# Performance work log

Hardware: AMD Instinct MI355X
Metric: run time of the kernel (lower is better)

## Reference

```python
import jax, jax.numpy as jnp
import numpy as np

N = 100000   # num nodes / num_embs
D = 64       # dim
E = 1200000  # num edges (before self-loops)
L = 2        # num_layers
H = 1        # heads
EPS = 1e-5
NEG_SLOPE = 0.2


def setup_inputs() -> dict:
    key = jax.random.key(0)
    ks = jax.random.split(key, 12)
    return {
        "x": jax.random.normal(ks[0], (N, D), jnp.float32),  # unused by forward (matches torch)
        "edge_index": jax.random.randint(ks[1], (2, E), 0, N, dtype=jnp.int64),
        "emb_weight": jax.random.normal(ks[2], (N, D), jnp.float32) * 0.1,
        "ln_gamma": jnp.ones((L, D), jnp.float32),
        "ln_beta": jnp.zeros((L, D), jnp.float32),
        "Wl": jax.random.normal(ks[3], (L, D, H * D), jnp.float32) * 0.05,
        "Wr": jax.random.normal(ks[4], (L, D, H * D), jnp.float32) * 0.05,
        "att": jax.random.normal(ks[5], (L, H, D), jnp.float32) * 0.05,
        "conv_bias": jnp.zeros((L, D), jnp.float32),
        "post_w": jax.random.normal(ks[6], (D, D), jnp.float32) * 0.05,
        "post_b": jnp.zeros((D,), jnp.float32),
    }


def _layernorm(x, g, b):
    # pyg LayerNorm(mode='node'): per-node normalization over features
    mu = jnp.mean(x, axis=-1, keepdims=True)
    var = jnp.var(x, axis=-1, keepdims=True)
    return (x - mu) * jax.lax.rsqrt(var + EPS) * g + b


def _gatv2(x, src, tgt, Wl, Wr, a, bias):
    # x: [N, D]; Wl/Wr: [D, H*D]; a: [H, D]
    xl = (x @ Wl).reshape(N, H, D)  # source transform
    xr = (x @ Wr).reshape(N, H, D)  # target transform
    m = jax.nn.leaky_relu(xl[src] + xr[tgt], NEG_SLOPE)      # [Et, H, D]
    e = jnp.einsum('ehd,hd->eh', m, a)                       # [Et, H]
    # segment softmax over edges grouped by target node
    emax = jax.ops.segment_max(e, tgt, num_segments=N)       # [N, H]
    ex = jnp.exp(e - emax[tgt])
    denom = jax.ops.segment_sum(ex, tgt, num_segments=N)
    alpha = ex / (denom[tgt] + 1e-16)                        # [Et, H]
    out = jax.ops.segment_sum(xl[src] * alpha[..., None], tgt, num_segments=N)  # [N, H, D]
    return out.mean(axis=1) + bias                           # concat=False -> mean over heads


def reference(x, edge_index, emb_weight, ln_gamma, ln_beta, Wl, Wr, att, conv_bias, post_w, post_b):
    # GATv2Conv default add_self_loops=True
    loops = jnp.arange(N, dtype=edge_index.dtype)
    src = jnp.concatenate([edge_index[0], loops])
    tgt = jnp.concatenate([edge_index[1], loops])
    h = emb_weight  # forward replaces input x with embedding table
    for i in range(L):
        y = _layernorm(h, ln_gamma[i], ln_beta[i])
        y = _gatv2(y, src, tgt, Wl[i], Wr[i], att[i], conv_bias[i])
        y = jax.nn.gelu(y, approximate=False)
        h = y + h  # residual
    return h @ post_w + post_b
```

## Files before the change

### kernel.cpp

```cpp
#include <hip/hip_runtime.h>
#include <math.h>

#define NN 100000
#define DD 64
#define NE 1200000
#define NB 391
#define SCH 2048
#define GB ((NN + 63) / 64)
#define HS 88

typedef __attribute__((ext_vector_type(8))) short bf16x8;
typedef __attribute__((ext_vector_type(4))) float f32x4;

__device__ __forceinline__ unsigned short f2bf(float x) {
    unsigned u = __float_as_uint(x);
    return (unsigned short)((u + 0x7FFFu + ((u >> 16) & 1u)) >> 16);
}
__device__ __forceinline__ float bf2f(unsigned short b) {
    return __uint_as_float(((unsigned)b) << 16);
}

__device__ __forceinline__ float gelu_exact(float x) {
    return 0.5f * x * (1.0f + erff(x * 0.70710678118654752f));
}

__device__ __forceinline__ float leaky(float x) {
    return fmaxf(x, 0.f) + 0.2f * fminf(x, 0.f);
}


__global__ __launch_bounds__(256) void k_bcount(const int* __restrict__ tgt, int* __restrict__ bcnt) {
    __shared__ int h[NB];
    for (int i = threadIdx.x; i < NB; i += 256) h[i] = 0;
    __syncthreads();
    const int stride = gridDim.x * 256;
    for (int i = blockIdx.x * 256 + threadIdx.x; i < NE; i += stride)
        atomicAdd(&h[tgt[i] >> 8], 1);
    __syncthreads();
    for (int i = threadIdx.x; i < NB; i += 256)
        if (h[i]) atomicAdd(&bcnt[i], h[i]);
}

__global__ __launch_bounds__(512) void k_bscan(const int* __restrict__ bcnt,
                                               int* __restrict__ bbase, int* __restrict__ wbase) {
    __shared__ int s[512];
    const int tid = threadIdx.x;
    const int v = (tid < NB) ? bcnt[tid] : 0;
    s[tid] = v;
    __syncthreads();
    for (int o = 1; o < 512; o <<= 1) {
        int t = (tid >= o) ? s[tid - o] : 0;
        __syncthreads();
        s[tid] += t;
        __syncthreads();
    }
    if (tid < NB) {
        int ex = s[tid] - v;
        bbase[tid] = ex;
        wbase[tid] = ex;
    }
    if (tid == NB - 1) bbase[NB] = s[tid];
}

__global__ __launch_bounds__(256) void k_bscatter(const int* __restrict__ src, const int* __restrict__ tgt,
                                                  int* __restrict__ wbase, unsigned int* __restrict__ ebuf) {
    __shared__ int stgt[SCH];
    __shared__ unsigned short srk[SCH];
    __shared__ int hist[NB];
    __shared__ int hbase[NB];
    const int base = blockIdx.x * SCH;
    const int cnt = min(SCH, NE - base);
    const int tid = threadIdx.x;
    for (int i = tid; i < NB; i += 256) hist[i] = 0;
    for (int i = tid; i < cnt; i += 256) stgt[i] = tgt[base + i];
    __syncthreads();
    for (int i = tid; i < cnt; i += 256)
        srk[i] = (unsigned short)atomicAdd(&hist[stgt[i] >> 8], 1);
    __syncthreads();
    for (int b = tid; b < NB; b += 256) {
        int c = hist[b];
        hbase[b] = c ? atomicAdd(&wbase[b], c) : 0;
    }
    __syncthreads();
    for (int i = tid; i < cnt; i += 256) {
        int t = stgt[i];
        unsigned int e = ((unsigned int)src[base + i] << 8) | (unsigned int)(t & 255);
        ebuf[hbase[t >> 8] + (int)srk[i]] = e;
    }
}

__global__ __launch_bounds__(256) void k_bfinal(const int* __restrict__ bbase,
                                                const unsigned int* __restrict__ ebuf,
                                                int* __restrict__ rowptr, int* __restrict__ csr) {
    __shared__ int hist[256];
    __shared__ int pos[256];
    __shared__ int wsum[4];
    const int b = blockIdx.x, tid = threadIdx.x;
    const int bb = bbase[b], be = bbase[b + 1];
    hist[tid] = 0;
    __syncthreads();
    for (int i = bb + tid; i < be; i += 256) atomicAdd(&hist[ebuf[i] & 255u], 1);
    __syncthreads();
    const int v = hist[tid];
    const int lane = tid & 63, w = tid >> 6;
    int sc = v;
    #pragma unroll
    for (int o = 1; o < 64; o <<= 1) { int t = __shfl_up(sc, o, 64); if (lane >= o) sc += t; }
    if (lane == 63) wsum[w] = sc;
    __syncthreads();
    int off = 0;
    for (int k = 0; k < w; ++k) off += wsum[k];
    const int node = b * 256 + tid;
    const int rp = bb + off + sc - v + node;
    if (node < NN) {
        rowptr[node] = rp;
        csr[rp] = node;
    } else if (node == NN) {
        rowptr[NN] = rp;
    }
    pos[tid] = rp + 1;
    __syncthreads();
    for (int i = bb + tid; i < be; i += 256) {
        unsigned int e = ebuf[i];
        int p = atomicAdd(&pos[e & 255u], 1);
        csr[p] = (int)(e >> 8);
    }
}

__global__ __launch_bounds__(128) void k_wprep(
    const float* __restrict__ Wl, const float* __restrict__ Wr,
    const float* __restrict__ g, const float* __restrict__ be,
    unsigned short* __restrict__ aT, float* __restrict__ S, float* __restrict__ C)
{
    const int c = threadIdx.x;
    const float* W = (c < 64) ? Wl : Wr;
    const int cc = c & 63;
    float s = 0.f, cC = 0.f;
    unsigned short* hi_p = aT + c * 64;
    unsigned short* lo_p = aT + 128 * 64 + c * 64;
    #pragma unroll 8
    for (int k = 0; k < 64; ++k) {
        float w = W[k * 64 + cc];
        float a = g[k] * w;
        unsigned short hi = f2bf(a);
        unsigned short lo = f2bf(a - bf2f(hi));
        hi_p[k] = hi; lo_p[k] = lo;
        s += a;
        cC = fmaf(be[k], w, cC);
    }
    S[c] = s; C[c] = cC;
}

__global__ __launch_bounds__(64) void k_wfinal(
    const float* __restrict__ pw, const float* __restrict__ pb,
    unsigned short* __restrict__ fT, float* __restrict__ Cf)
{
    const int c = threadIdx.x;
    unsigned short* hi_p = fT + c * 64;
    unsigned short* lo_p = fT + 64 * 64 + c * 64;
    #pragma unroll 8
    for (int k = 0; k < 64; ++k) {
        float w = pw[k * 64 + c];
        unsigned short hi = f2bf(w);
        unsigned short lo = f2bf(w - bf2f(hi));
        hi_p[k] = hi; lo_p[k] = lo;
    }
    Cf[c] = pb[c];
}

template<int CTW, bool LN>
__global__ __launch_bounds__(256) void k_gemm(
    const float* __restrict__ h, const unsigned short* __restrict__ aT,
    const float* __restrict__ S, const float* __restrict__ C,
    float* __restrict__ xl, float* __restrict__ xr, float* __restrict__ outp)
{
    __shared__ __align__(16) unsigned short hbh[64 * HS];
    __shared__ __align__(16) unsigned short hbl[64 * HS];
    __shared__ float smean[64], srho[64];
    const int tid = threadIdx.x;
    const int tile = blockIdx.x * 64;
    {
        const int row = tid >> 2, q = tid & 3;
        const int node = min(tile + row, NN - 1);
        const float* hp = h + (size_t)node * DD + q * 16;
        float4 v[4];
        #pragma unroll
        for (int i = 0; i < 4; ++i) v[i] = *(const float4*)(hp + i * 4);
        if (LN) {
            float sum = 0.f, ssq = 0.f;
            #pragma unroll
            for (int i = 0; i < 4; ++i) {
                sum += v[i].x + v[i].y + v[i].z + v[i].w;
                ssq += v[i].x * v[i].x + v[i].y * v[i].y + v[i].z * v[i].z + v[i].w * v[i].w;
            }
            sum += __shfl_xor(sum, 1, 64); ssq += __shfl_xor(ssq, 1, 64);
            sum += __shfl_xor(sum, 2, 64); ssq += __shfl_xor(ssq, 2, 64);
            if (q == 0) {
                float mean = sum * 0.015625f;
                float var = ssq * 0.015625f - mean * mean;
                smean[row] = mean;
                srho[row] = rsqrtf(var + 1e-5f);
            }
        }
        #pragma unroll
        for (int half = 0; half < 2; ++half) {
            bf16x8 ph, pl;
            #pragma unroll
            for (int e = 0; e < 8; ++e) {
                float f = (&v[half * 2 + (e >> 2)].x)[e & 3];
                unsigned short hi = f2bf(f);
                unsigned short lo = f2bf(f - bf2f(hi));
                ph[e] = (short)hi; pl[e] = (short)lo;
            }
            const int so = row * HS + q * 16 + half * 8;
            *(bf16x8*)&hbh[so] = ph;
            *(bf16x8*)&hbl[so] = pl;
        }
    }
    __syncthreads();
    const int lane = tid & 63;
    const int wslot = tid >> 6;
    const int li16 = lane & 15;
    const int g16 = lane >> 4;
    const int NCT = CTW * 4;
    f32x4 acc[CTW][4];
    #pragma unroll
    for (int c = 0; c < CTW; ++c)
        #pragma unroll
        for (int rt = 0; rt < 4; ++rt) acc[c][rt] = (f32x4){0.f, 0.f, 0.f, 0.f};
    #pragma unroll
    for (int kk = 0; kk < 2; ++kk) {
        bf16x8 ah[4], al[4];
        #pragma unroll
        for (int rt = 0; rt < 4; ++rt) {
            const int so = (rt * 16 + li16) * HS + kk * 32 + g16 * 8;
            ah[rt] = *(const bf16x8*)&hbh[so];
            al[rt] = *(const bf16x8*)&hbl[so];
        }
        #pragma unroll
        for (int c = 0; c < CTW; ++c) {
            const int ct = wslot + c * 4;
            const unsigned short* bp = aT + (ct * 16 + li16) * 64 + kk * 32 + g16 * 8;
            bf16x8 bh = *(const bf16x8*)bp;
            bf16x8 bl = *(const bf16x8*)(bp + NCT * 16 * 64);
            #pragma unroll
            for (int rt = 0; rt < 4; ++rt) {
                acc[c][rt] = __builtin_amdgcn_mfma_f32_16x16x32_bf16(ah[rt], bh, acc[c][rt], 0, 0, 0);
                acc[c][rt] = __builtin_amdgcn_mfma_f32_16x16x32_bf16(al[rt], bh, acc[c][rt], 0, 0, 0);
                acc[c][rt] = __builtin_amdgcn_mfma_f32_16x16x32_bf16(ah[rt], bl, acc[c][rt], 0, 0, 0);
            }
        }
    }
    #pragma unroll
    for (int c = 0; c < CTW; ++c) {
        const int ct = wslot + c * 4;
        const int col = ct * 16 + li16;
        const float Cc = C[col];
        float Sc = 0.f;
        if (LN) Sc = S[col];
        float* xb;
        int cc;
        if (LN) { xb = (ct < 4) ? xl : xr; cc = col & 63; }
        else    { xb = outp; cc = col; }
        #pragma unroll
        for (int rt = 0; rt < 4; ++rt) {
            const int r0 = rt * 16 + g16 * 4;
            #pragma unroll
            for (int j = 0; j < 4; ++j) {
                const int row2 = r0 + j;
                const int node = tile + row2;
                if (node < NN) {
                    float p = acc[c][rt][j];
                    float val;
                    if (LN) val = fmaf(srho[row2], p - smean[row2] * Sc, Cc);
                    else    val = p + Cc;
                    xb[(size_t)node * DD + cc] = val;
                }
            }
        }
    }
}

__global__ __launch_bounds__(256) void k_agg(
    const int* __restrict__ rowptr, const int* __restrict__ csr,
    const float* __restrict__ xl, const float* __restrict__ xr,
    const float* __restrict__ att, const float* __restrict__ cbias,
    const float* __restrict__ h_in, float* __restrict__ h_out)
{
    const int lane = threadIdx.x & 63;
    const int li   = lane & 15;
    const int sub  = lane >> 4;
    const int wid  = (blockIdx.x * 256 + threadIdx.x) >> 6;
    const int nw   = gridDim.x * 4;
    const float4 a4  = *(const float4*)&att[li * 4];
    const float4 cb4 = *(const float4*)&cbias[li * 4];
    for (int n = wid; n < NN; n += nw) {
        const float4 xrt = *(const float4*)&xr[(size_t)n * DD + li * 4];
        const int beg = rowptr[n], end = rowptr[n + 1];
        const int end1 = end - 1;
        int j  = beg + sub;
        int jc = min(j, end1);
        int s  = csr[jc];
        float4 v = *(const float4*)&xl[(size_t)s * DD + li * 4];
        float  den = 0.f;
        float4 acc = make_float4(0.f, 0.f, 0.f, 0.f);
        const int nch = (end - beg + 3) >> 2;
        for (int c = 0; c < nch; ++c) {
            float4 cur = v;
            const int jcur = j;
            j += 4;
            jc = min(j, end1);
            s  = csr[jc];
            v  = *(const float4*)&xl[(size_t)s * DD + li * 4];
            float p = leaky(cur.x + xrt.x) * a4.x;
            p = fmaf(leaky(cur.y + xrt.y), a4.y, p);
            p = fmaf(leaky(cur.z + xrt.z), a4.z, p);
            p = fmaf(leaky(cur.w + xrt.w), a4.w, p);
            p += __shfl_xor(p, 1, 64);
            p += __shfl_xor(p, 2, 64);
            p += __shfl_xor(p, 4, 64);
            p += __shfl_xor(p, 8, 64);
            float ex = (jcur < end) ? __expf(p) : 0.f;
            den += ex;
            acc.x = fmaf(ex, cur.x, acc.x);
            acc.y = fmaf(ex, cur.y, acc.y);
            acc.z = fmaf(ex, cur.z, acc.z);
            acc.w = fmaf(ex, cur.w, acc.w);
        }
        #pragma unroll
        for (int o = 16; o < 64; o <<= 1) {
            acc.x += __shfl_xor(acc.x, o, 64);
            acc.y += __shfl_xor(acc.y, o, 64);
            acc.z += __shfl_xor(acc.z, o, 64);
            acc.w += __shfl_xor(acc.w, o, 64);
            den   += __shfl_xor(den,   o, 64);
        }
        if (sub == 0) {
            const float id = 1.f / (den + 1e-16f);
            const float4 hi = *(const float4*)&h_in[(size_t)n * DD + li * 4];
            float4 o4;
            o4.x = gelu_exact(fmaf(acc.x, id, cb4.x)) + hi.x;
            o4.y = gelu_exact(fmaf(acc.y, id, cb4.y)) + hi.y;
            o4.z = gelu_exact(fmaf(acc.z, id, cb4.z)) + hi.z;
            o4.w = gelu_exact(fmaf(acc.w, id, cb4.w)) + hi.w;
            *(float4*)&h_out[(size_t)n * DD + li * 4] = o4;
        }
    }
}

extern "C" void kernel_launch(void* const* d_in, const int* in_sizes, int n_in,
                              void* d_out, int out_size, void* d_ws, size_t ws_size,
                              hipStream_t stream) {
    const int*   edge_index = (const int*)d_in[1];
    const int*   src   = edge_index;
    const int*   tgt   = edge_index + NE;
    const float* emb   = (const float*)d_in[2];
    const float* ln_g  = (const float*)d_in[3];
    const float* ln_b  = (const float*)d_in[4];
    const float* Wl    = (const float*)d_in[5];
    const float* Wr    = (const float*)d_in[6];
    const float* att   = (const float*)d_in[7];
    const float* cbias = (const float*)d_in[8];
    const float* pw    = (const float*)d_in[9];
    const float* pb    = (const float*)d_in[10];
    float* out = (float*)d_out;

    float* xl = (float*)d_ws;
    float* xr = xl + (size_t)NN * DD;
    int* csr             = (int*)(xr + (size_t)NN * DD);
    unsigned int* ebuf   = (unsigned int*)(csr + NE + NN);
    int* rowptr          = (int*)(ebuf + NE);
    int* bcnt            = rowptr + NN + 8;
    int* bbase           = bcnt + 392;
    int* wbase           = bbase + 400;
    unsigned short* aT0  = (unsigned short*)(wbase + 400);
    unsigned short* aT1  = aT0 + 2 * 128 * 64;
    unsigned short* fT   = aT1 + 2 * 128 * 64;
    float* S0 = (float*)(fT + 2 * 64 * 64);
    float* C0 = S0 + 128;
    float* S1 = C0 + 128;
    float* C1 = S1 + 128;
    float* Cf = C1 + 128;

    const int AGG_BLOCKS = 2048;

    k_wprep<<<1, 128, 0, stream>>>(Wl, Wr, ln_g, ln_b, aT0, S0, C0);
    k_wprep<<<1, 128, 0, stream>>>(Wl + DD * DD, Wr + DD * DD, ln_g + DD, ln_b + DD, aT1, S1, C1);
    k_wfinal<<<1, 64, 0, stream>>>(pw, pb, fT, Cf);

    hipMemsetAsync(bcnt, 0, NB * sizeof(int), stream);
    k_bcount<<<256, 256, 0, stream>>>(tgt, bcnt);
    k_bscan<<<1, 512, 0, stream>>>(bcnt, bbase, wbase);
    k_bscatter<<<(NE + SCH - 1) / SCH, 256, 0, stream>>>(src, tgt, wbase, ebuf);
    k_bfinal<<<NB, 256, 0, stream>>>(bbase, ebuf, rowptr, csr);

    k_gemm<2, true><<<GB, 256, 0, stream>>>(emb, aT0, S0, C0, xl, xr, nullptr);
    k_agg<<<AGG_BLOCKS, 256, 0, stream>>>(rowptr, csr, xl, xr, att, cbias, emb, out);

    k_gemm<2, true><<<GB, 256, 0, stream>>>(out, aT1, S1, C1, xl, xr, nullptr);
    k_agg<<<AGG_BLOCKS, 256, 0, stream>>>(rowptr, csr, xl, xr, att + DD, cbias + DD, out, out);

    k_gemm<1, false><<<GB, 256, 0, stream>>>(out, fT, nullptr, Cf, nullptr, nullptr, out);
}
```

Before: 266.9 us.

## Store source-transformed features xl in bf16 and gather 8 edges per wave

```diff
diff --git a/kernel.cpp b/kernel.cpp
--- a/kernel.cpp
+++ b/kernel.cpp
@@ -172,7 +172,7 @@
 __global__ __launch_bounds__(256) void k_gemm(
     const float* __restrict__ h, const unsigned short* __restrict__ aT,
     const float* __restrict__ S, const float* __restrict__ C,
-    float* __restrict__ xl, float* __restrict__ xr, float* __restrict__ outp)
+    unsigned short* __restrict__ xlb, float* __restrict__ xr, float* __restrict__ outp)
 {
     __shared__ __align__(16) unsigned short hbh[64 * HS];
     __shared__ __align__(16) unsigned short hbl[64 * HS];
@@ -258,10 +258,6 @@
         const float Cc = C[col];
         float Sc = 0.f;
         if (LN) Sc = S[col];
-        float* xb;
-        int cc;
-        if (LN) { xb = (ct < 4) ? xl : xr; cc = col & 63; }
-        else    { xb = outp; cc = col; }
         #pragma unroll
         for (int rt = 0; rt < 4; ++rt) {
             const int r0 = rt * 16 + g16 * 4;
@@ -271,10 +267,13 @@
                 const int node = tile + row2;
                 if (node < NN) {
                     float p = acc[c][rt][j];
-                    float val;
-                    if (LN) val = fmaf(srho[row2], p - smean[row2] * Sc, Cc);
-                    else    val = p + Cc;
-                    xb[(size_t)node * DD + cc] = val;
+                    if (LN) {
+                        float val = fmaf(srho[row2], p - smean[row2] * Sc, Cc);
+                        if (ct < 4) xlb[(size_t)node * DD + col]       = f2bf(val);
+                        else        xr[(size_t)node * DD + (col & 63)] = val;
+                    } else {
+                        outp[(size_t)node * DD + col] = p + Cc;
+                    }
                 }
             }
         }
@@ -283,67 +282,82 @@
 
 __global__ __launch_bounds__(256) void k_agg(
     const int* __restrict__ rowptr, const int* __restrict__ csr,
-    const float* __restrict__ xl, const float* __restrict__ xr,
+    const unsigned short* __restrict__ xlb, const float* __restrict__ xr,
     const float* __restrict__ att, const float* __restrict__ cbias,
     const float* __restrict__ h_in, float* __restrict__ h_out)
 {
     const int lane = threadIdx.x & 63;
-    const int li   = lane & 15;
-    const int sub  = lane >> 4;
+    const int li   = lane & 7;
+    const int sub  = lane >> 3;
     const int wid  = (blockIdx.x * 256 + threadIdx.x) >> 6;
     const int nw   = gridDim.x * 4;
-    const float4 a4  = *(const float4*)&att[li * 4];
-    const float4 cb4 = *(const float4*)&cbias[li * 4];
+    float a[8], xrt[8];
+    {
+        const float4 a0 = *(const float4*)&att[li * 8];
+        const float4 a1 = *(const float4*)&att[li * 8 + 4];
+        a[0]=a0.x; a[1]=a0.y; a[2]=a0.z; a[3]=a0.w;
+        a[4]=a1.x; a[5]=a1.y; a[6]=a1.z; a[7]=a1.w;
+    }
+    const float4 cb0 = *(const float4*)&cbias[li * 8];
+    const float4 cb1 = *(const float4*)&cbias[li * 8 + 4];
     for (int n = wid; n < NN; n += nw) {
-        const float4 xrt = *(const float4*)&xr[(size_t)n * DD + li * 4];
+        {
+            const float4 x0 = *(const float4*)&xr[(size_t)n * DD + li * 8];
+            const float4 x1 = *(const float4*)&xr[(size_t)n * DD + li * 8 + 4];
+            xrt[0]=x0.x; xrt[1]=x0.y; xrt[2]=x0.z; xrt[3]=x0.w;
+            xrt[4]=x1.x; xrt[5]=x1.y; xrt[6]=x1.z; xrt[7]=x1.w;
+        }
         const int beg = rowptr[n], end = rowptr[n + 1];
         const int end1 = end - 1;
         int j  = beg + sub;
         int jc = min(j, end1);
         int s  = csr[jc];
-        float4 v = *(const float4*)&xl[(size_t)s * DD + li * 4];
+        bf16x8 v = *(const bf16x8*)&xlb[(size_t)s * DD + li * 8];
         float  den = 0.f;
-        float4 acc = make_float4(0.f, 0.f, 0.f, 0.f);
-        const int nch = (end - beg + 3) >> 2;
+        float  acc[8] = {0.f,0.f,0.f,0.f,0.f,0.f,0.f,0.f};
+        const int nch = (end - beg + 7) >> 3;
         for (int c = 0; c < nch; ++c) {
-            float4 cur = v;
+            bf16x8 curp = v;
             const int jcur = j;
-            j += 4;
+            j += 8;
             jc = min(j, end1);
             s  = csr[jc];
-            v  = *(const float4*)&xl[(size_t)s * DD + li * 4];
-            float p = leaky(cur.x + xrt.x) * a4.x;
-            p = fmaf(leaky(cur.y + xrt.y), a4.y, p);
-            p = fmaf(leaky(cur.z + xrt.z), a4.z, p);
-            p = fmaf(leaky(cur.w + xrt.w), a4.w, p);
+            v  = *(const bf16x8*)&xlb[(size_t)s * DD + li * 8];
+            float f[8];
+            #pragma unroll
+            for (int i = 0; i < 8; ++i) f[i] = bf2f((unsigned short)curp[i]);
+            float p = leaky(f[0] + xrt[0]) * a[0];
+            #pragma unroll
+            for (int i = 1; i < 8; ++i) p = fmaf(leaky(f[i] + xrt[i]), a[i], p);
             p += __shfl_xor(p, 1, 64);
             p += __shfl_xor(p, 2, 64);
             p += __shfl_xor(p, 4, 64);
-            p += __shfl_xor(p, 8, 64);
             float ex = (jcur < end) ? __expf(p) : 0.f;
             den += ex;
-            acc.x = fmaf(ex, cur.x, acc.x);
-            acc.y = fmaf(ex, cur.y, acc.y);
-            acc.z = fmaf(ex, cur.z, acc.z);
-            acc.w = fmaf(ex, cur.w, acc.w);
-        }
-        #pragma unroll
-        for (int o = 16; o < 64; o <<= 1) {
-            acc.x += __shfl_xor(acc.x, o, 64);
-            acc.y += __shfl_xor(acc.y, o, 64);
-            acc.z += __shfl_xor(acc.z, o, 64);
-            acc.w += __shfl_xor(acc.w, o, 64);
-            den   += __shfl_xor(den,   o, 64);
+            #pragma unroll
+            for (int i = 0; i < 8; ++i) acc[i] = fmaf(ex, f[i], acc[i]);
+        }
+        #pragma unroll
+        for (int o = 8; o < 64; o <<= 1) {
+            #pragma unroll
+            for (int i = 0; i < 8; ++i) acc[i] += __shfl_xor(acc[i], o, 64);
+            den += __shfl_xor(den, o, 64);
         }
         if (sub == 0) {
             const float id = 1.f / (den + 1e-16f);
-            const float4 hi = *(const float4*)&h_in[(size_t)n * DD + li * 4];
-            float4 o4;
-            o4.x = gelu_exact(fmaf(acc.x, id, cb4.x)) + hi.x;
-            o4.y = gelu_exact(fmaf(acc.y, id, cb4.y)) + hi.y;
-            o4.z = gelu_exact(fmaf(acc.z, id, cb4.z)) + hi.z;
-            o4.w = gelu_exact(fmaf(acc.w, id, cb4.w)) + hi.w;
-            *(float4*)&h_out[(size_t)n * DD + li * 4] = o4;
+            const float4 hi0 = *(const float4*)&h_in[(size_t)n * DD + li * 8];
+            const float4 hi1 = *(const float4*)&h_in[(size_t)n * DD + li * 8 + 4];
+            float4 o0, o1;
+            o0.x = gelu_exact(fmaf(acc[0], id, cb0.x)) + hi0.x;
+            o0.y = gelu_exact(fmaf(acc[1], id, cb0.y)) + hi0.y;
+            o0.z = gelu_exact(fmaf(acc[2], id, cb0.z)) + hi0.z;
+            o0.w = gelu_exact(fmaf(acc[3], id, cb0.w)) + hi0.w;
+            o1.x = gelu_exact(fmaf(acc[4], id, cb1.x)) + hi1.x;
+            o1.y = gelu_exact(fmaf(acc[5], id, cb1.y)) + hi1.y;
+            o1.z = gelu_exact(fmaf(acc[6], id, cb1.z)) + hi1.z;
+            o1.w = gelu_exact(fmaf(acc[7], id, cb1.w)) + hi1.w;
+            *(float4*)&h_out[(size_t)n * DD + li * 8]     = o0;
+            *(float4*)&h_out[(size_t)n * DD + li * 8 + 4] = o1;
         }
     }
 }
@@ -365,8 +379,8 @@
     const float* pb    = (const float*)d_in[10];
     float* out = (float*)d_out;
 
-    float* xl = (float*)d_ws;
-    float* xr = xl + (size_t)NN * DD;
+    unsigned short* xlb = (unsigned short*)d_ws;
+    float* xr = (float*)(xlb + (size_t)NN * DD);
     int* csr             = (int*)(xr + (size_t)NN * DD);
     unsigned int* ebuf   = (unsigned int*)(csr + NE + NN);
     int* rowptr          = (int*)(ebuf + NE);
@@ -394,11 +408,11 @@
     k_bscatter<<<(NE + SCH - 1) / SCH, 256, 0, stream>>>(src, tgt, wbase, ebuf);
     k_bfinal<<<NB, 256, 0, stream>>>(bbase, ebuf, rowptr, csr);
 
-    k_gemm<2, true><<<GB, 256, 0, stream>>>(emb, aT0, S0, C0, xl, xr, nullptr);
-    k_agg<<<AGG_BLOCKS, 256, 0, stream>>>(rowptr, csr, xl, xr, att, cbias, emb, out);
-
-    k_gemm<2, true><<<GB, 256, 0, stream>>>(out, aT1, S1, C1, xl, xr, nullptr);
-    k_agg<<<AGG_BLOCKS, 256, 0, stream>>>(rowptr, csr, xl, xr, att + DD, cbias + DD, out, out);
+    k_gemm<2, true><<<GB, 256, 0, stream>>>(emb, aT0, S0, C0, xlb, xr, nullptr);
+    k_agg<<<AGG_BLOCKS, 256, 0, stream>>>(rowptr, csr, xlb, xr, att, cbias, emb, out);
+
+    k_gemm<2, true><<<GB, 256, 0, stream>>>(out, aT1, S1, C1, xlb, xr, nullptr);
+    k_agg<<<AGG_BLOCKS, 256, 0, stream>>>(rowptr, csr, xlb, xr, att + DD, cbias + DD, out, out);
 
     k_gemm<1, false><<<GB, 256, 0, stream>>>(out, fT, nullptr, Cf, nullptr, nullptr, out);
 }
```

Result: slower. 296.0 us (+10.9%).

## Store source-transformed features in bf16 and deepen gather prefetch in aggregation

Applied to the files above, without the earlier changes.

```diff
diff --git a/kernel.cpp b/kernel.cpp
--- a/kernel.cpp
+++ b/kernel.cpp
@@ -172,7 +172,7 @@
 __global__ __launch_bounds__(256) void k_gemm(
     const float* __restrict__ h, const unsigned short* __restrict__ aT,
     const float* __restrict__ S, const float* __restrict__ C,
-    float* __restrict__ xl, float* __restrict__ xr, float* __restrict__ outp)
+    unsigned short* __restrict__ xlb, float* __restrict__ xr, float* __restrict__ outp)
 {
     __shared__ __align__(16) unsigned short hbh[64 * HS];
     __shared__ __align__(16) unsigned short hbl[64 * HS];
@@ -258,10 +258,6 @@
         const float Cc = C[col];
         float Sc = 0.f;
         if (LN) Sc = S[col];
-        float* xb;
-        int cc;
-        if (LN) { xb = (ct < 4) ? xl : xr; cc = col & 63; }
-        else    { xb = outp; cc = col; }
         #pragma unroll
         for (int rt = 0; rt < 4; ++rt) {
             const int r0 = rt * 16 + g16 * 4;
@@ -271,10 +267,13 @@
                 const int node = tile + row2;
                 if (node < NN) {
                     float p = acc[c][rt][j];
-                    float val;
-                    if (LN) val = fmaf(srho[row2], p - smean[row2] * Sc, Cc);
-                    else    val = p + Cc;
-                    xb[(size_t)node * DD + cc] = val;
+                    if (LN) {
+                        float val = fmaf(srho[row2], p - smean[row2] * Sc, Cc);
+                        if (ct < 4) xlb[(size_t)node * DD + col]       = f2bf(val);
+                        else        xr[(size_t)node * DD + (col & 63)] = val;
+                    } else {
+                        outp[(size_t)node * DD + col] = p + Cc;
+                    }
                 }
             }
         }
@@ -283,7 +282,7 @@
 
 __global__ __launch_bounds__(256) void k_agg(
     const int* __restrict__ rowptr, const int* __restrict__ csr,
-    const float* __restrict__ xl, const float* __restrict__ xr,
+    const unsigned short* __restrict__ xlb, const float* __restrict__ xr,
     const float* __restrict__ att, const float* __restrict__ cbias,
     const float* __restrict__ h_in, float* __restrict__ h_out)
 {
@@ -299,33 +298,37 @@
         const int beg = rowptr[n], end = rowptr[n + 1];
         const int end1 = end - 1;
         int j  = beg + sub;
-        int jc = min(j, end1);
-        int s  = csr[jc];
-        float4 v = *(const float4*)&xl[(size_t)s * DD + li * 4];
+        int jn = j + 4;
+        int s0 = csr[min(j,  end1)];
+        ushort4 v  = *(const ushort4*)&xlb[(size_t)s0 * DD + li * 4];
+        int s1 = csr[min(jn, end1)];
+        ushort4 vn = *(const ushort4*)&xlb[(size_t)s1 * DD + li * 4];
         float  den = 0.f;
         float4 acc = make_float4(0.f, 0.f, 0.f, 0.f);
         const int nch = (end - beg + 3) >> 2;
         for (int c = 0; c < nch; ++c) {
-            float4 cur = v;
+            const ushort4 cur = v;
             const int jcur = j;
-            j += 4;
-            jc = min(j, end1);
-            s  = csr[jc];
-            v  = *(const float4*)&xl[(size_t)s * DD + li * 4];
-            float p = leaky(cur.x + xrt.x) * a4.x;
-            p = fmaf(leaky(cur.y + xrt.y), a4.y, p);
-            p = fmaf(leaky(cur.z + xrt.z), a4.z, p);
-            p = fmaf(leaky(cur.w + xrt.w), a4.w, p);
+            v = vn;
+            j = jn;
+            jn += 4;
+            int s2 = csr[min(jn, end1)];
+            vn = *(const ushort4*)&xlb[(size_t)s2 * DD + li * 4];
+            float f0 = bf2f(cur.x), f1 = bf2f(cur.y), f2 = bf2f(cur.z), f3 = bf2f(cur.w);
+            float p = leaky(f0 + xrt.x) * a4.x;
+            p = fmaf(leaky(f1 + xrt.y), a4.y, p);
+            p = fmaf(leaky(f2 + xrt.z), a4.z, p);
+            p = fmaf(leaky(f3 + xrt.w), a4.w, p);
             p += __shfl_xor(p, 1, 64);
             p += __shfl_xor(p, 2, 64);
             p += __shfl_xor(p, 4, 64);
             p += __shfl_xor(p, 8, 64);
             float ex = (jcur < end) ? __expf(p) : 0.f;
             den += ex;
-            acc.x = fmaf(ex, cur.x, acc.x);
-            acc.y = fmaf(ex, cur.y, acc.y);
-            acc.z = fmaf(ex, cur.z, acc.z);
-            acc.w = fmaf(ex, cur.w, acc.w);
+            acc.x = fmaf(ex, f0, acc.x);
+            acc.y = fmaf(ex, f1, acc.y);
+            acc.z = fmaf(ex, f2, acc.z);
+            acc.w = fmaf(ex, f3, acc.w);
         }
         #pragma unroll
         for (int o = 16; o < 64; o <<= 1) {
@@ -365,8 +368,8 @@
     const float* pb    = (const float*)d_in[10];
     float* out = (float*)d_out;
 
-    float* xl = (float*)d_ws;
-    float* xr = xl + (size_t)NN * DD;
+    unsigned short* xlb = (unsigned short*)d_ws;
+    float* xr = (float*)(xlb + (size_t)NN * DD);
     int* csr             = (int*)(xr + (size_t)NN * DD);
     unsigned int* ebuf   = (unsigned int*)(csr + NE + NN);
     int* rowptr          = (int*)(ebuf + NE);
@@ -394,11 +397,11 @@
     k_bscatter<<<(NE + SCH - 1) / SCH, 256, 0, stream>>>(src, tgt, wbase, ebuf);
     k_bfinal<<<NB, 256, 0, stream>>>(bbase, ebuf, rowptr, csr);
 
-    k_gemm<2, true><<<GB, 256, 0, stream>>>(emb, aT0, S0, C0, xl, xr, nullptr);
-    k_agg<<<AGG_BLOCKS, 256, 0, stream>>>(rowptr, csr, xl, xr, att, cbias, emb, out);
-
-    k_gemm<2, true><<<GB, 256, 0, stream>>>(out, aT1, S1, C1, xl, xr, nullptr);
-    k_agg<<<AGG_BLOCKS, 256, 0, stream>>>(rowptr, csr, xl, xr, att + DD, cbias + DD, out, out);
+    k_gemm<2, true><<<GB, 256, 0, stream>>>(emb, aT0, S0, C0, xlb, xr, nullptr);
+    k_agg<<<AGG_BLOCKS, 256, 0, stream>>>(rowptr, csr, xlb, xr, att, cbias, emb, out);
+
+    k_gemm<2, true><<<GB, 256, 0, stream>>>(out, aT1, S1, C1, xlb, xr, nullptr);
+    k_agg<<<AGG_BLOCKS, 256, 0, stream>>>(rowptr, csr, xlb, xr, att + DD, cbias + DD, out, out);
 
     k_gemm<1, false><<<GB, 256, 0, stream>>>(out, fT, nullptr, Cf, nullptr, nullptr, out);
 }
```

Result: faster. 260.8 us (-2.3%).
